# Kernel optimization log

Measured on AMD Instinct MI355X. Metric: run time of the kernel, lower is better.

The kernel has to match this reference:

```python
import jax, jax.numpy as jnp
import numpy as np
from jax import lax

EPS = 1e-5

def _conv3x3(x, w, stride=1):
    # x: [B,C,H,W], w: [O,I,3,3]
    dn = lax.conv_dimension_numbers(x.shape, w.shape, ('NCHW', 'OIHW', 'NCHW'))
    return lax.conv_general_dilated(x, w, window_strides=(stride, stride),
                                    padding=((1, 1), (1, 1)), dimension_numbers=dn)

def _batchnorm(x, gamma, beta):
    # training-mode BN over (N,H,W) per channel
    mean = jnp.mean(x, axis=(0, 2, 3), keepdims=True)
    var = jnp.var(x, axis=(0, 2, 3), keepdims=True)
    inv = lax.rsqrt(var + EPS)
    return (x - mean) * inv * gamma[None, :, None, None] + beta[None, :, None, None]

def setup_inputs() -> dict:
    key = jax.random.key(0)
    ks = jax.random.split(key, 8)
    B, C, H, W, E = 16, 256, 64, 64, 512
    x = jax.random.normal(ks[0], (B, C, H, W), dtype=jnp.float32)
    embedding = jax.random.normal(ks[1], (B, E), dtype=jnp.float32)
    s_conv = 1.0 / np.sqrt(C * 9)
    conv1_w = jax.random.normal(ks[2], (C, C, 3, 3), dtype=jnp.float32) * s_conv
    conv2_w = jax.random.normal(ks[3], (C, C, 3, 3), dtype=jnp.float32) * s_conv
    s_g = 1.0 / np.sqrt(E)
    g1_w = jax.random.normal(ks[4], (E, C), dtype=jnp.float32) * s_g
    g1_b = jnp.zeros((C,), dtype=jnp.float32)
    g2_w = jax.random.normal(ks[5], (E, C), dtype=jnp.float32) * s_g
    g2_b = jnp.zeros((C,), dtype=jnp.float32)
    bn1_g = jnp.ones((C,), dtype=jnp.float32)
    bn1_b = jnp.zeros((C,), dtype=jnp.float32)
    bn2_g = jnp.ones((C,), dtype=jnp.float32)
    bn2_b = jnp.zeros((C,), dtype=jnp.float32)
    return {"x": x, "embedding": embedding, "conv1_w": conv1_w, "conv2_w": conv2_w,
            "g1_w": g1_w, "g1_b": g1_b, "g2_w": g2_w, "g2_b": g2_b,
            "bn1_g": bn1_g, "bn1_b": bn1_b, "bn2_g": bn2_g, "bn2_b": bn2_b}

def reference(x, embedding, conv1_w, conv2_w, g1_w, g1_b, g2_w, g2_b,
              bn1_g, bn1_b, bn2_g, bn2_b):
    identity = x
    # gate 1: per-sample per-channel gate values (softmax over channels)
    gate1 = jax.nn.softmax(embedding @ g1_w + g1_b, axis=-1)  # [B,C]
    out = _conv3x3(x, conv1_w, stride=1) * gate1[:, :, None, None]
    out = jax.nn.relu(_batchnorm(out, bn1_g, bn1_b))
    # gate 2
    gate2 = jax.nn.softmax(embedding @ g2_w + g2_b, axis=-1)  # [B,C]
    out = _conv3x3(out, conv2_w, stride=1) * gate2[:, :, None, None]
    out = _batchnorm(out, bn2_g, bn2_b)
    out = jax.nn.relu(out + identity)
    return (out, gate1, gate2)
```

## Files before the change

kernel.cpp:

```cpp
#include <hip/hip_runtime.h>

typedef __attribute__((ext_vector_type(8))) short short8;
typedef __attribute__((ext_vector_type(4))) float f32x4;

#define HP 66

__device__ __forceinline__ unsigned short f2bf(float f) {
  unsigned u = __builtin_bit_cast(unsigned, f);
  u += 0x7FFFu + ((u >> 16) & 1u);
  return (unsigned short)(u >> 16);
}
__device__ __forceinline__ float bf2f(unsigned short h) {
  return __builtin_bit_cast(float, ((unsigned)h) << 16);
}
__device__ __forceinline__ __attribute__((address_space(3))) void* to_as3(void* p) {
  return (__attribute__((address_space(3))) void*)(unsigned)(unsigned long long)p;
}
__device__ __forceinline__ const __attribute__((address_space(1))) void* to_as1(const void* p) {
  return (const __attribute__((address_space(1))) void*)(unsigned long long)p;
}

#define SB0() __builtin_amdgcn_sched_barrier(0)
#define BAR() do { SB0(); __builtin_amdgcn_s_barrier(); SB0(); } while (0)

__global__ __launch_bounds__(256) void k_prep(
    const float* __restrict__ x, unsigned short* __restrict__ xp,
    const float* __restrict__ w1, const float* __restrict__ w2,
    unsigned short* __restrict__ wT1, unsigned short* __restrict__ wT2,
    const float* __restrict__ emb,
    const float* __restrict__ g1w, const float* __restrict__ g1b,
    const float* __restrict__ g2w, const float* __restrict__ g2b,
    float* __restrict__ gate1, float* __restrict__ gate2) {
  __shared__ float tile[32][65];
  __shared__ float ebuf[512];
  __shared__ float red[8];
  const int blk = blockIdx.x;
  const int t = threadIdx.x;

  if (blk < 8192) {
    int ct = blk & 7, h = (blk >> 3) & 63, b = blk >> 9;
    int c0 = ct * 32;
    int w = t & 63, cs = t >> 6;
#pragma unroll
    for (int i = 0; i < 8; ++i) {
      int c = cs + i * 4;
      tile[c][w] = x[(((b * 256) + c0 + c) * 64 + h) * 64 + w];
    }
    __syncthreads();
    int cl = (t & 15) * 2, w0 = t >> 4;
#pragma unroll
    for (int i = 0; i < 4; ++i) {
      int ww = w0 + i * 16;
      unsigned v = (unsigned)f2bf(tile[cl][ww]) | ((unsigned)f2bf(tile[cl + 1][ww]) << 16);
      *(unsigned*)(xp + ((long)((b*HP + h + 1)*HP + (ww + 1)) * 256 + c0 + cl)) = v;
    }
  } else if (blk < 10272) {
    unsigned u = (unsigned)(blk - 8192) * 256 + t;
    unsigned p_idx = u >> 7, word = u & 127;
    int img = p_idx / 260, p = p_idx % 260;
    int h, w;
    if (p < 66)      { h = 0;  w = p; }
    else if (p < 132){ h = 65; w = p - 66; }
    else             { int q = p - 132; h = 1 + (q >> 1); w = (q & 1) * 65; }
    ((unsigned*)xp)[((long)((img*HP + h)*HP + w) * 256) / 2 + word] = 0u;
  } else if (blk < 10784) {
    int idx = blk - 10272;
    const float* w = (idx >> 8) ? w2 : w1;
    unsigned short* wT = (idx >> 8) ? wT2 : wT1;
    int co = idx & 255;
#pragma unroll
    for (int kk = 0; kk < 9; ++kk)
      wT[co * 2304 + kk * 256 + t] = f2bf(w[(co * 256 + t) * 9 + kk]);
  } else {
    int idx = blk - 10784;
    int b = idx & 15;
    const float* gw = (idx >> 4) ? g2w : g1w;
    const float* gbias = (idx >> 4) ? g2b : g1b;
    float* gout = (idx >> 4) ? gate2 : gate1;
    ebuf[t] = emb[b * 512 + t];
    ebuf[t + 256] = emb[b * 512 + t + 256];
    __syncthreads();
    float acc = gbias[t];
    for (int k = 0; k < 512; ++k) acc += ebuf[k] * gw[k * 256 + t];
    float mx = acc;
    for (int off = 32; off >= 1; off >>= 1) mx = fmaxf(mx, __shfl_xor(mx, off));
    if ((t & 63) == 0) red[t >> 6] = mx;
    __syncthreads();
    mx = fmaxf(fmaxf(red[0], red[1]), fmaxf(red[2], red[3]));
    float e = expf(acc - mx);
    float sm = e;
    for (int off = 32; off >= 1; off >>= 1) sm += __shfl_xor(sm, off);
    if ((t & 63) == 0) red[4 + (t >> 6)] = sm;
    __syncthreads();
    sm = red[4] + red[5] + red[6] + red[7];
    gout[b * 256 + t] = e / sm;
  }
}

__global__ __launch_bounds__(512, 2) void k_conv(
    const unsigned short* __restrict__ inp,
    const unsigned short* __restrict__ wT,
    const float* __restrict__ gate,
    unsigned short* __restrict__ yout,
    float* __restrict__ partials) {
  __shared__ short As[2][256][64];
  __shared__ short Bs[2][256][64];
  __shared__ float sbuf[2][256][2];

  const int t = threadIdx.x;
  const int lane = t & 63;
  const int wid = t >> 6;
  const int wm = wid >> 2;
  const int wn = wid & 3;
  const int lr = lane & 15;
  const int hi = lane >> 4;
  const int key = lr & 7;

  const int blk = ((blockIdx.x & 7) << 5) + (blockIdx.x >> 3);
  const int b = blk >> 4;
  const int hh4 = (blk & 15) << 2;

  const int r0 = t >> 3;
  const int cdst = (t & 7) << 3;
  const int cg8 = (((t & 7) ^ ((t >> 3) & 7)) << 3);

  int aoff[4];
#pragma unroll
  for (int i = 0; i < 4; ++i)
    aoff[i] = (b * HP + hh4 + i) * HP + r0;

  auto stageA = [&](int buf, int half, int s) {
    int kk = s >> 2;
    int kh = (kk * 11) >> 5;
    int khw = kh * 66 + (kk - kh * 3);
    int ci = ((s & 3) << 6) + cg8;
    const unsigned short* g0 = inp + (long)(aoff[half * 2 + 0] + khw) * 256 + ci;
    const unsigned short* g1 = inp + (long)(aoff[half * 2 + 1] + khw) * 256 + ci;
    __builtin_amdgcn_global_load_lds(to_as1(g0), to_as3((void*)&As[buf][half * 128 + r0][cdst]), 16, 0, 0);
    __builtin_amdgcn_global_load_lds(to_as1(g1), to_as3((void*)&As[buf][half * 128 + 64 + r0][cdst]), 16, 0, 0);
  };
  auto stageB = [&](int buf, int half, int s) {
    int co0 = half * 128 + r0;
    const unsigned short* g0 = wT + (long)co0 * 2304 + s * 64 + cg8;
    const unsigned short* g1 = wT + (long)(co0 + 64) * 2304 + s * 64 + cg8;
    __builtin_amdgcn_global_load_lds(to_as1(g0), to_as3((void*)&Bs[buf][half * 128 + r0][cdst]), 16, 0, 0);
    __builtin_amdgcn_global_load_lds(to_as1(g1), to_as3((void*)&Bs[buf][half * 128 + 64 + r0][cdst]), 16, 0, 0);
  };

  f32x4 acc[8][4];
#pragma unroll
  for (int i = 0; i < 8; ++i)
#pragma unroll
    for (int j = 0; j < 4; ++j) acc[i][j] = (f32x4){0.f, 0.f, 0.f, 0.f};

  short8 afrag0[4][2], afrag1[4][2];
  short8 bfrag0[2][2], bfrag1[2][2];

#define RD_A(ARR, MH, BUF)                                                           \
  _Pragma("unroll") for (int mf = 0; mf < 4; ++mf)                                   \
    _Pragma("unroll") for (int ks = 0; ks < 2; ++ks)                                 \
      ARR[mf][ks] = *(const short8*)&As[BUF][wm * 128 + ((MH) * 4 + mf) * 16 + lr][((ks * 4 + hi) ^ key) << 3];
#define RD_B(ARR, NH, BUF)                                                           \
  _Pragma("unroll") for (int nf = 0; nf < 2; ++nf)                                   \
    _Pragma("unroll") for (int ks = 0; ks < 2; ++ks)                                 \
      ARR[nf][ks] = *(const short8*)&Bs[BUF][wn * 64 + ((NH) * 2 + nf) * 16 + lr][((ks * 4 + hi) ^ key) << 3];

#define QUADQ(AF, BF, mh, nh)                                                        \
  do {                                                                               \
    __builtin_amdgcn_s_setprio(1);                                                   \
    _Pragma("unroll") for (int ks = 0; ks < 2; ++ks)                                 \
      _Pragma("unroll") for (int mo = 0; mo < 4; ++mo)                               \
        _Pragma("unroll") for (int no = 0; no < 2; ++no)                             \
          acc[(mh) * 4 + mo][(nh) * 2 + no] = __builtin_amdgcn_mfma_f32_16x16x32_bf16( \
              AF[mo][ks], BF[no][ks], acc[(mh) * 4 + mo][(nh) * 2 + no], 0, 0, 0);   \
    __builtin_amdgcn_s_setprio(0);                                                   \
  } while (0)

  stageA(0, 0, 0); stageB(0, 0, 0); stageA(0, 1, 0); stageB(0, 1, 0);
  stageA(1, 0, 1); stageB(1, 0, 1); stageA(1, 1, 1); stageB(1, 1, 1);
  asm volatile("s_waitcnt vmcnt(8)" ::: "memory");
  BAR();
  RD_B(bfrag0, 0, 0);
  RD_A(afrag0, 0, 0);

#define KTHALF2(SEL, kt)                                                             \
  {                                                                                  \
    RD_B(bfrag1, 1, SEL);                                                            \
    RD_A(afrag1, 1, SEL);                                                            \
    SB0();                                                                           \
    QUADQ(afrag0, bfrag0, 0, 0);                                                     \
    QUADQ(afrag0, bfrag1, 0, 1);                                                     \
    QUADQ(afrag1, bfrag0, 1, 0);                                                     \
    if ((kt) < 35) { asm volatile("s_waitcnt vmcnt(4)" ::: "memory"); }              \
    BAR();                                                                           \
    if ((kt) < 35) { RD_B(bfrag0, 0, SEL ^ 1); RD_A(afrag0, 0, SEL ^ 1); }           \
    if ((kt) + 2 < 36) { stageA(SEL, 0, (kt) + 2); stageB(SEL, 0, (kt) + 2);         \
                         stageA(SEL, 1, (kt) + 2); stageB(SEL, 1, (kt) + 2); }       \
    SB0();                                                                           \
    QUADQ(afrag1, bfrag1, 1, 1);                                                     \
    if ((kt) < 34)      { asm volatile("s_waitcnt vmcnt(8)" ::: "memory"); }         \
    else if ((kt) == 34){ asm volatile("s_waitcnt vmcnt(0)" ::: "memory"); }         \
    BAR();                                                                           \
  }

  for (int i = 0; i < 18; ++i) {
    const int kt0 = 2 * i;
    KTHALF2(0, kt0)
    KTHALF2(1, kt0 + 1)
  }
#undef KTHALF2
#undef QUADQ
#undef RD_A
#undef RD_B

  float g[4];
#pragma unroll
  for (int nf = 0; nf < 4; ++nf) g[nf] = gate[(b << 8) + wn * 64 + nf * 16 + lr];

  float s[4] = {0, 0, 0, 0}, sq[4] = {0, 0, 0, 0};
  const int mrow0 = (blk << 8) + wm * 128 + (hi << 2);
  const int c0 = wn * 64 + lr;
#pragma unroll
  for (int mf = 0; mf < 8; ++mf)
#pragma unroll
    for (int r = 0; r < 4; ++r) {
      const int mm = mrow0 + mf * 16 + r;
#pragma unroll
      for (int nf = 0; nf < 4; ++nf) {
        float v = acc[mf][nf][r] * g[nf];
        yout[(long)mm * 256 + c0 + nf * 16] = f2bf(v);
        s[nf] += v;
        sq[nf] += v * v;
      }
    }
#pragma unroll
  for (int nf = 0; nf < 4; ++nf) {
    s[nf] += __shfl_xor(s[nf], 16);  s[nf] += __shfl_xor(s[nf], 32);
    sq[nf] += __shfl_xor(sq[nf], 16); sq[nf] += __shfl_xor(sq[nf], 32);
  }
  if (hi == 0) {
#pragma unroll
    for (int nf = 0; nf < 4; ++nf) {
      int c = wn * 64 + nf * 16 + lr;
      sbuf[wm][c][0] = s[nf];
      sbuf[wm][c][1] = sq[nf];
    }
  }
  __syncthreads();
  if (t < 256) {
    partials[((blk << 8) + t) * 2]     = sbuf[0][t][0] + sbuf[1][t][0];
    partials[((blk << 8) + t) * 2 + 1] = sbuf[0][t][1] + sbuf[1][t][1];
  }
}

__global__ __launch_bounds__(256) void k_bnfin(const float* __restrict__ partials,
                                               const float* __restrict__ gamma,
                                               const float* __restrict__ beta,
                                               float2* __restrict__ aff) {
  __shared__ float red[8];
  int c = blockIdx.x, t = threadIdx.x;
  float s = partials[(t * 256 + c) * 2];
  float sq = partials[(t * 256 + c) * 2 + 1];
  for (int off = 32; off >= 1; off >>= 1) { s += __shfl_xor(s, off); sq += __shfl_xor(sq, off); }
  if ((t & 63) == 0) { red[t >> 6] = s; red[4 + (t >> 6)] = sq; }
  __syncthreads();
  if (t == 0) {
    s = red[0] + red[1] + red[2] + red[3];
    sq = red[4] + red[5] + red[6] + red[7];
    float mean = s * (1.0f / 65536.0f);
    float var = fmaxf(sq * (1.0f / 65536.0f) - mean * mean, 0.0f);
    float inv = rsqrtf(var + 1e-5f);
    float ga = gamma[c] * inv;
    aff[c] = make_float2(ga, beta[c] - mean * ga);
  }
}

__global__ __launch_bounds__(256) void k_mid(const unsigned short* __restrict__ y1,
                                             const float2* __restrict__ aff,
                                             unsigned short* __restrict__ zp) {
  long idx = (long)blockIdx.x * 256 + threadIdx.x;
  int c0 = (int)(idx & 31) * 8;
  long pos = idx >> 5;
  int b = (int)(pos >> 12), hw = (int)(pos & 4095);
  int h = hw >> 6, w = hw & 63;
  uint4 v = *(const uint4*)(y1 + pos * 256 + c0);
  unsigned vv[4] = {v.x, v.y, v.z, v.w};
  unsigned outp[4];
#pragma unroll
  for (int j = 0; j < 4; ++j) {
    float2 aL = aff[c0 + 2 * j], aH = aff[c0 + 2 * j + 1];
    float lo = fmaxf(aL.x * bf2f((unsigned short)(vv[j] & 0xFFFF)) + aL.y, 0.f);
    float hiv = fmaxf(aH.x * bf2f((unsigned short)(vv[j] >> 16)) + aH.y, 0.f);
    outp[j] = (unsigned)f2bf(lo) | ((unsigned)f2bf(hiv) << 16);
  }
  unsigned short* dst = zp + (long)((b * HP + h + 1) * HP + w + 1) * 256 + c0;
  *(uint4*)dst = make_uint4(outp[0], outp[1], outp[2], outp[3]);
}

__global__ __launch_bounds__(256) void k_final(const unsigned short* __restrict__ y2,
                                               const float2* __restrict__ aff,
                                               const float* __restrict__ x,
                                               float* __restrict__ out) {
  __shared__ float tile[64][33];
  int blk = blockIdx.x;
  int ct = blk & 7, h = (blk >> 3) & 63, b = blk >> 9;
  int c0 = ct * 32;
  int t = threadIdx.x;
  int cl = (t & 15) * 2, w0 = t >> 4;
#pragma unroll
  for (int i = 0; i < 4; ++i) {
    int w = w0 + i * 16;
    unsigned v = *(const unsigned*)(y2 + (long)((b * 4096) + h * 64 + w) * 256 + c0 + cl);
    float2 aL = aff[c0 + cl], aH = aff[c0 + cl + 1];
    tile[w][cl] = aL.x * bf2f((unsigned short)(v & 0xFFFF)) + aL.y;
    tile[w][cl + 1] = aH.x * bf2f((unsigned short)(v >> 16)) + aH.y;
  }
  __syncthreads();
  int w = t & 63, csub = t >> 6;
#pragma unroll
  for (int j = 0; j < 8; ++j) {
    int c = c0 + csub * 8 + j;
    long o = ((long)(b * 256 + c) * 64 + h) * 64 + w;
    out[o] = fmaxf(tile[w][csub * 8 + j] + x[o], 0.f);
  }
}

extern "C" void kernel_launch(void* const* d_in, const int* in_sizes, int n_in,
                              void* d_out, int out_size, void* d_ws, size_t ws_size,
                              hipStream_t stream) {
  const float* x    = (const float*)d_in[0];
  const float* emb  = (const float*)d_in[1];
  const float* w1   = (const float*)d_in[2];
  const float* w2   = (const float*)d_in[3];
  const float* g1w  = (const float*)d_in[4];
  const float* g1b  = (const float*)d_in[5];
  const float* g2w  = (const float*)d_in[6];
  const float* g2b  = (const float*)d_in[7];
  const float* bn1g = (const float*)d_in[8];
  const float* bn1b = (const float*)d_in[9];
  const float* bn2g = (const float*)d_in[10];
  const float* bn2b = (const float*)d_in[11];

  float* out = (float*)d_out;
  float* gate1 = out + 16777216;
  float* gate2 = gate1 + 4096;

  char* ws = (char*)d_ws;
  const size_t OFF_XP  = 0;
  const size_t OFF_WT1 = 35684352;
  const size_t OFF_WT2 = OFF_WT1 + 1179648;
  const size_t OFF_Y   = OFF_WT2 + 1179648;
  const size_t OFF_PART = OFF_Y + 33554432;
  const size_t OFF_AFF1 = OFF_PART + 1048576;
  const size_t OFF_AFF2 = OFF_AFF1 + 2048;

  unsigned short* xp  = (unsigned short*)(ws + OFF_XP);
  unsigned short* wT1 = (unsigned short*)(ws + OFF_WT1);
  unsigned short* wT2 = (unsigned short*)(ws + OFF_WT2);
  unsigned short* y   = (unsigned short*)(ws + OFF_Y);
  float* part = (float*)(ws + OFF_PART);
  float2* aff1 = (float2*)(ws + OFF_AFF1);
  float2* aff2 = (float2*)(ws + OFF_AFF2);

  k_prep<<<10816, 256, 0, stream>>>(x, xp, w1, w2, wT1, wT2, emb,
                                    g1w, g1b, g2w, g2b, gate1, gate2);

  k_conv<<<256, 512, 0, stream>>>(xp, wT1, gate1, y, part);
  k_bnfin<<<256, 256, 0, stream>>>(part, bn1g, bn1b, aff1);
  k_mid<<<8192, 256, 0, stream>>>(y, aff1, xp);

  k_conv<<<256, 512, 0, stream>>>(xp, wT2, gate2, y, part);
  k_bnfin<<<256, 256, 0, stream>>>(part, bn2g, bn2b, aff2);
  k_final<<<8192, 256, 0, stream>>>(y, aff2, x, out);
}
```

Before: 213.5 us.

## Restructure GEMM main loop into barrier-separated phases with interleaved staging

Replaces the two-half K-tile loop with an eight-phase schedule per pair of K-steps. Each phase reads one quadrant's fragments, issues part of the next stage's global-to-LDS loads, then runs 16 MFMAs, with a barrier and an lgkmcnt wait between phases. The A and B staging is remapped by row halves so that each load only overwrites LDS rows already consumed in earlier phases. A single A-fragment buffer replaces the double buffer to lower register use. The intent is finer overlap of loads and LDS reads with MFMA work, at the cost of many more barriers and stricter lockstep between waves.

Measured after the change: 216.6 us. No clear change (+1.4%).

```diff
diff --git a/kernel.cpp b/kernel.cpp
--- a/kernel.cpp
+++ b/kernel.cpp
@@ -129,22 +129,22 @@
   for (int i = 0; i < 4; ++i)
     aoff[i] = (b * HP + hh4 + i) * HP + r0;
 
-  auto stageA = [&](int buf, int half, int s) {
+  auto stageA_h = [&](int buf, int h, int s) {
     int kk = s >> 2;
     int kh = (kk * 11) >> 5;
     int khw = kh * 66 + (kk - kh * 3);
     int ci = ((s & 3) << 6) + cg8;
-    const unsigned short* g0 = inp + (long)(aoff[half * 2 + 0] + khw) * 256 + ci;
-    const unsigned short* g1 = inp + (long)(aoff[half * 2 + 1] + khw) * 256 + ci;
-    __builtin_amdgcn_global_load_lds(to_as1(g0), to_as3((void*)&As[buf][half * 128 + r0][cdst]), 16, 0, 0);
-    __builtin_amdgcn_global_load_lds(to_as1(g1), to_as3((void*)&As[buf][half * 128 + 64 + r0][cdst]), 16, 0, 0);
+    const unsigned short* g0 = inp + (long)(aoff[h] + khw) * 256 + ci;
+    const unsigned short* g1 = inp + (long)(aoff[h + 2] + khw) * 256 + ci;
+    __builtin_amdgcn_global_load_lds(to_as1(g0), to_as3((void*)&As[buf][h * 64 + r0][cdst]), 16, 0, 0);
+    __builtin_amdgcn_global_load_lds(to_as1(g1), to_as3((void*)&As[buf][h * 64 + 128 + r0][cdst]), 16, 0, 0);
   };
-  auto stageB = [&](int buf, int half, int s) {
-    int co0 = half * 128 + r0;
-    const unsigned short* g0 = wT + (long)co0 * 2304 + s * 64 + cg8;
-    const unsigned short* g1 = wT + (long)(co0 + 64) * 2304 + s * 64 + cg8;
-    __builtin_amdgcn_global_load_lds(to_as1(g0), to_as3((void*)&Bs[buf][half * 128 + r0][cdst]), 16, 0, 0);
-    __builtin_amdgcn_global_load_lds(to_as1(g1), to_as3((void*)&Bs[buf][half * 128 + 64 + r0][cdst]), 16, 0, 0);
+  auto stageB_h = [&](int buf, int h, int s) {
+    int rB = (r0 & 31) + ((r0 >> 5) << 6) + h * 32;
+    const unsigned short* g0 = wT + (long)rB * 2304 + s * 64 + cg8;
+    const unsigned short* g1 = wT + (long)(rB + 128) * 2304 + s * 64 + cg8;
+    __builtin_amdgcn_global_load_lds(to_as1(g0), to_as3((void*)&Bs[buf][rB][cdst]), 16, 0, 0);
+    __builtin_amdgcn_global_load_lds(to_as1(g1), to_as3((void*)&Bs[buf][rB + 128][cdst]), 16, 0, 0);
   };
 
   f32x4 acc[8][4];
@@ -153,62 +153,82 @@
 #pragma unroll
     for (int j = 0; j < 4; ++j) acc[i][j] = (f32x4){0.f, 0.f, 0.f, 0.f};
 
-  short8 afrag0[4][2], afrag1[4][2];
+  short8 afrag[4][2];
   short8 bfrag0[2][2], bfrag1[2][2];
 
-#define RD_A(ARR, MH, BUF)                                                           \
+#define RD_A(MH, BUF)                                                                \
   _Pragma("unroll") for (int mf = 0; mf < 4; ++mf)                                   \
     _Pragma("unroll") for (int ks = 0; ks < 2; ++ks)                                 \
-      ARR[mf][ks] = *(const short8*)&As[BUF][wm * 128 + ((MH) * 4 + mf) * 16 + lr][((ks * 4 + hi) ^ key) << 3];
+      afrag[mf][ks] = *(const short8*)&As[BUF][wm * 128 + (MH) * 64 + mf * 16 + lr][((ks * 4 + hi) ^ key) << 3];
 #define RD_B(ARR, NH, BUF)                                                           \
   _Pragma("unroll") for (int nf = 0; nf < 2; ++nf)                                   \
     _Pragma("unroll") for (int ks = 0; ks < 2; ++ks)                                 \
       ARR[nf][ks] = *(const short8*)&Bs[BUF][wn * 64 + ((NH) * 2 + nf) * 16 + lr][((ks * 4 + hi) ^ key) << 3];
 
-#define QUADQ(AF, BF, mh, nh)                                                        \
+#define QUADQ(BF, mh, nh)                                                            \
   do {                                                                               \
     __builtin_amdgcn_s_setprio(1);                                                   \
     _Pragma("unroll") for (int ks = 0; ks < 2; ++ks)                                 \
       _Pragma("unroll") for (int mo = 0; mo < 4; ++mo)                               \
         _Pragma("unroll") for (int no = 0; no < 2; ++no)                             \
           acc[(mh) * 4 + mo][(nh) * 2 + no] = __builtin_amdgcn_mfma_f32_16x16x32_bf16( \
-              AF[mo][ks], BF[no][ks], acc[(mh) * 4 + mo][(nh) * 2 + no], 0, 0, 0);   \
+              afrag[mo][ks], BF[no][ks], acc[(mh) * 4 + mo][(nh) * 2 + no], 0, 0, 0); \
     __builtin_amdgcn_s_setprio(0);                                                   \
   } while (0)
 
-  stageA(0, 0, 0); stageB(0, 0, 0); stageA(0, 1, 0); stageB(0, 1, 0);
-  stageA(1, 0, 1); stageB(1, 0, 1); stageA(1, 1, 1); stageB(1, 1, 1);
+#define LGKM0() do { asm volatile("s_waitcnt lgkmcnt(0)" ::: "memory"); SB0(); } while (0)
+
+  stageA_h(0, 0, 0); stageB_h(0, 0, 0); stageA_h(0, 1, 0); stageB_h(0, 1, 0);
+  stageA_h(1, 0, 1); stageB_h(1, 0, 1); stageA_h(1, 1, 1); stageB_h(1, 1, 1);
   asm volatile("s_waitcnt vmcnt(8)" ::: "memory");
   BAR();
-  RD_B(bfrag0, 0, 0);
-  RD_A(afrag0, 0, 0);
-
-#define KTHALF2(SEL, kt)                                                             \
-  {                                                                                  \
-    RD_B(bfrag1, 1, SEL);                                                            \
-    RD_A(afrag1, 1, SEL);                                                            \
-    SB0();                                                                           \
-    QUADQ(afrag0, bfrag0, 0, 0);                                                     \
-    QUADQ(afrag0, bfrag1, 0, 1);                                                     \
-    QUADQ(afrag1, bfrag0, 1, 0);                                                     \
-    if ((kt) < 35) { asm volatile("s_waitcnt vmcnt(4)" ::: "memory"); }              \
-    BAR();                                                                           \
-    if ((kt) < 35) { RD_B(bfrag0, 0, SEL ^ 1); RD_A(afrag0, 0, SEL ^ 1); }           \
-    if ((kt) + 2 < 36) { stageA(SEL, 0, (kt) + 2); stageB(SEL, 0, (kt) + 2);         \
-                         stageA(SEL, 1, (kt) + 2); stageB(SEL, 1, (kt) + 2); }       \
-    SB0();                                                                           \
-    QUADQ(afrag1, bfrag1, 1, 1);                                                     \
-    if ((kt) < 34)      { asm volatile("s_waitcnt vmcnt(8)" ::: "memory"); }         \
-    else if ((kt) == 34){ asm volatile("s_waitcnt vmcnt(0)" ::: "memory"); }         \
-    BAR();                                                                           \
-  }
 
   for (int i = 0; i < 18; ++i) {
-    const int kt0 = 2 * i;
-    KTHALF2(0, kt0)
-    KTHALF2(1, kt0 + 1)
-  }
-#undef KTHALF2
+    const int s2 = 2 * i + 2;
+    const int s3 = 2 * i + 3;
+    const bool g2q = (s2 < 36), g3q = (s3 < 36);
+    RD_B(bfrag0, 0, 0);
+    RD_A(0, 0);
+    BAR(); LGKM0();
+    QUADQ(bfrag0, 0, 0);
+    BAR();
+    RD_B(bfrag1, 1, 0);
+    if (g2q) stageA_h(0, 0, s2);
+    BAR(); LGKM0();
+    QUADQ(bfrag1, 0, 1);
+    BAR();
+    RD_A(1, 0);
+    if (g2q) stageB_h(0, 0, s2);
+    BAR(); LGKM0();
+    QUADQ(bfrag1, 1, 1);
+    BAR();
+    if (g2q) { stageA_h(0, 1, s2); stageB_h(0, 1, s2); }
+    BAR(); LGKM0();
+    QUADQ(bfrag0, 1, 0);
+    asm volatile("s_waitcnt vmcnt(8)" ::: "memory");
+    BAR();
+    RD_B(bfrag0, 0, 1);
+    RD_A(0, 1);
+    BAR(); LGKM0();
+    QUADQ(bfrag0, 0, 0);
+    BAR();
+    RD_B(bfrag1, 1, 1);
+    if (g3q) stageA_h(1, 0, s3);
+    BAR(); LGKM0();
+    QUADQ(bfrag1, 0, 1);
+    BAR();
+    RD_A(1, 1);
+    if (g3q) stageB_h(1, 0, s3);
+    BAR(); LGKM0();
+    QUADQ(bfrag1, 1, 1);
+    BAR();
+    if (g3q) { stageA_h(1, 1, s3); stageB_h(1, 1, s3); }
+    BAR(); LGKM0();
+    QUADQ(bfrag0, 1, 0);
+    asm volatile("s_waitcnt vmcnt(8)" ::: "memory");
+    BAR();
+  }
+#undef LGKM0
 #undef QUADQ
 #undef RD_A
 #undef RD_B
```

## Shrink conv tiles to 128x128 with 256-thread blocks and 1024-block grid

Applied to the files above, without the earlier changes.

Implicit-GEMM conv tile changes from 256x256 per 512-thread block to 128x128 per 256-thread block, splitting output channels into two halves. The grid grows from 256 to 1024 blocks. This is meant to fill all 256 CUs with several blocks each instead of one block per CU, which should improve latency hiding and occupancy. The partials layout is rearranged into separate sum and sum-of-squares planes, and the BN finalize kernel now reduces 512 tiles. The trade-off is that the smaller tiles reuse less data, so each block does more global and LDS traffic per FLOP.

Result: slower. 238.1 us (+11.5%).

```diff
diff --git a/kernel.cpp b/kernel.cpp
--- a/kernel.cpp
+++ b/kernel.cpp
@@ -97,28 +97,30 @@
   }
 }
 
-__global__ __launch_bounds__(512, 2) void k_conv(
+__global__ __launch_bounds__(256, 2) void k_conv(
     const unsigned short* __restrict__ inp,
     const unsigned short* __restrict__ wT,
     const float* __restrict__ gate,
     unsigned short* __restrict__ yout,
     float* __restrict__ partials) {
-  __shared__ short As[2][256][64];
-  __shared__ short Bs[2][256][64];
-  __shared__ float sbuf[2][256][2];
+  __shared__ short As[2][128][64];
+  __shared__ short Bs[2][128][64];
+  __shared__ float sbuf[2][128][2];
 
   const int t = threadIdx.x;
   const int lane = t & 63;
   const int wid = t >> 6;
-  const int wm = wid >> 2;
-  const int wn = wid & 3;
+  const int wm = wid >> 1;
+  const int wn = wid & 1;
   const int lr = lane & 15;
   const int hi = lane >> 4;
   const int key = lr & 7;
 
-  const int blk = ((blockIdx.x & 7) << 5) + (blockIdx.x >> 3);
-  const int b = blk >> 4;
-  const int hh4 = (blk & 15) << 2;
+  const int blk = ((blockIdx.x & 7) << 7) + (blockIdx.x >> 3);
+  const int mt = blk >> 1;
+  const int nt = blk & 1;
+  const int b = mt >> 5;
+  const int hh2 = (mt & 31) << 1;
 
   const int r0 = t >> 3;
   const int cdst = (t & 7) << 3;
@@ -127,57 +129,57 @@
   int aoff[4];
 #pragma unroll
   for (int i = 0; i < 4; ++i)
-    aoff[i] = (b * HP + hh4 + i) * HP + r0;
-
-  auto stageA = [&](int buf, int half, int s) {
+    aoff[i] = (b * HP + hh2 + (i >> 1)) * HP + (r0 + 32 * (i & 1));
+
+  auto stageA_h = [&](int buf, int h, int s) {
     int kk = s >> 2;
     int kh = (kk * 11) >> 5;
     int khw = kh * 66 + (kk - kh * 3);
     int ci = ((s & 3) << 6) + cg8;
-    const unsigned short* g0 = inp + (long)(aoff[half * 2 + 0] + khw) * 256 + ci;
-    const unsigned short* g1 = inp + (long)(aoff[half * 2 + 1] + khw) * 256 + ci;
-    __builtin_amdgcn_global_load_lds(to_as1(g0), to_as3((void*)&As[buf][half * 128 + r0][cdst]), 16, 0, 0);
-    __builtin_amdgcn_global_load_lds(to_as1(g1), to_as3((void*)&As[buf][half * 128 + 64 + r0][cdst]), 16, 0, 0);
+    const unsigned short* g0 = inp + (long)(aoff[h] + khw) * 256 + ci;
+    const unsigned short* g1 = inp + (long)(aoff[2 + h] + khw) * 256 + ci;
+    __builtin_amdgcn_global_load_lds(to_as1(g0), to_as3((void*)&As[buf][h * 32 + r0][cdst]), 16, 0, 0);
+    __builtin_amdgcn_global_load_lds(to_as1(g1), to_as3((void*)&As[buf][64 + h * 32 + r0][cdst]), 16, 0, 0);
   };
-  auto stageB = [&](int buf, int half, int s) {
-    int co0 = half * 128 + r0;
-    const unsigned short* g0 = wT + (long)co0 * 2304 + s * 64 + cg8;
-    const unsigned short* g1 = wT + (long)(co0 + 64) * 2304 + s * 64 + cg8;
-    __builtin_amdgcn_global_load_lds(to_as1(g0), to_as3((void*)&Bs[buf][half * 128 + r0][cdst]), 16, 0, 0);
-    __builtin_amdgcn_global_load_lds(to_as1(g1), to_as3((void*)&Bs[buf][half * 128 + 64 + r0][cdst]), 16, 0, 0);
+  auto stageB_h = [&](int buf, int h, int s) {
+    int co = nt * 128 + h * 32 + r0;
+    const unsigned short* g0 = wT + (long)co * 2304 + s * 64 + cg8;
+    const unsigned short* g1 = wT + (long)(co + 64) * 2304 + s * 64 + cg8;
+    __builtin_amdgcn_global_load_lds(to_as1(g0), to_as3((void*)&Bs[buf][h * 32 + r0][cdst]), 16, 0, 0);
+    __builtin_amdgcn_global_load_lds(to_as1(g1), to_as3((void*)&Bs[buf][64 + h * 32 + r0][cdst]), 16, 0, 0);
   };
 
-  f32x4 acc[8][4];
-#pragma unroll
-  for (int i = 0; i < 8; ++i)
+  f32x4 acc[4][4];
+#pragma unroll
+  for (int i = 0; i < 4; ++i)
 #pragma unroll
     for (int j = 0; j < 4; ++j) acc[i][j] = (f32x4){0.f, 0.f, 0.f, 0.f};
 
-  short8 afrag0[4][2], afrag1[4][2];
+  short8 afrag0[2][2], afrag1[2][2];
   short8 bfrag0[2][2], bfrag1[2][2];
 
-#define RD_A(ARR, MH, BUF)                                                           \
-  _Pragma("unroll") for (int mf = 0; mf < 4; ++mf)                                   \
+#define RD_A(ARR, AH, BUF)                                                           \
+  _Pragma("unroll") for (int mf = 0; mf < 2; ++mf)                                   \
     _Pragma("unroll") for (int ks = 0; ks < 2; ++ks)                                 \
-      ARR[mf][ks] = *(const short8*)&As[BUF][wm * 128 + ((MH) * 4 + mf) * 16 + lr][((ks * 4 + hi) ^ key) << 3];
+      ARR[mf][ks] = *(const short8*)&As[BUF][wm * 64 + (AH) * 32 + mf * 16 + lr][((ks * 4 + hi) ^ key) << 3];
 #define RD_B(ARR, NH, BUF)                                                           \
   _Pragma("unroll") for (int nf = 0; nf < 2; ++nf)                                   \
     _Pragma("unroll") for (int ks = 0; ks < 2; ++ks)                                 \
-      ARR[nf][ks] = *(const short8*)&Bs[BUF][wn * 64 + ((NH) * 2 + nf) * 16 + lr][((ks * 4 + hi) ^ key) << 3];
+      ARR[nf][ks] = *(const short8*)&Bs[BUF][wn * 64 + (NH) * 32 + nf * 16 + lr][((ks * 4 + hi) ^ key) << 3];
 
 #define QUADQ(AF, BF, mh, nh)                                                        \
   do {                                                                               \
     __builtin_amdgcn_s_setprio(1);                                                   \
     _Pragma("unroll") for (int ks = 0; ks < 2; ++ks)                                 \
-      _Pragma("unroll") for (int mo = 0; mo < 4; ++mo)                               \
+      _Pragma("unroll") for (int mo = 0; mo < 2; ++mo)                               \
         _Pragma("unroll") for (int no = 0; no < 2; ++no)                             \
-          acc[(mh) * 4 + mo][(nh) * 2 + no] = __builtin_amdgcn_mfma_f32_16x16x32_bf16( \
-              AF[mo][ks], BF[no][ks], acc[(mh) * 4 + mo][(nh) * 2 + no], 0, 0, 0);   \
+          acc[(mh) * 2 + mo][(nh) * 2 + no] = __builtin_amdgcn_mfma_f32_16x16x32_bf16( \
+              AF[mo][ks], BF[no][ks], acc[(mh) * 2 + mo][(nh) * 2 + no], 0, 0, 0);   \
     __builtin_amdgcn_s_setprio(0);                                                   \
   } while (0)
 
-  stageA(0, 0, 0); stageB(0, 0, 0); stageA(0, 1, 0); stageB(0, 1, 0);
-  stageA(1, 0, 1); stageB(1, 0, 1); stageA(1, 1, 1); stageB(1, 1, 1);
+  stageA_h(0, 0, 0); stageB_h(0, 0, 0); stageA_h(0, 1, 0); stageB_h(0, 1, 0);
+  stageA_h(1, 0, 1); stageB_h(1, 0, 1); stageA_h(1, 1, 1); stageB_h(1, 1, 1);
   asm volatile("s_waitcnt vmcnt(8)" ::: "memory");
   BAR();
   RD_B(bfrag0, 0, 0);
@@ -194,8 +196,8 @@
     if ((kt) < 35) { asm volatile("s_waitcnt vmcnt(4)" ::: "memory"); }              \
     BAR();                                                                           \
     if ((kt) < 35) { RD_B(bfrag0, 0, SEL ^ 1); RD_A(afrag0, 0, SEL ^ 1); }           \
-    if ((kt) + 2 < 36) { stageA(SEL, 0, (kt) + 2); stageB(SEL, 0, (kt) + 2);         \
-                         stageA(SEL, 1, (kt) + 2); stageB(SEL, 1, (kt) + 2); }       \
+    if ((kt) + 2 < 36) { stageA_h(SEL, 0, (kt) + 2); stageB_h(SEL, 0, (kt) + 2);     \
+                         stageA_h(SEL, 1, (kt) + 2); stageB_h(SEL, 1, (kt) + 2); }   \
     SB0();                                                                           \
     QUADQ(afrag1, bfrag1, 1, 1);                                                     \
     if ((kt) < 34)      { asm volatile("s_waitcnt vmcnt(8)" ::: "memory"); }         \
@@ -215,13 +217,14 @@
 
   float g[4];
 #pragma unroll
-  for (int nf = 0; nf < 4; ++nf) g[nf] = gate[(b << 8) + wn * 64 + nf * 16 + lr];
+  for (int nf = 0; nf < 4; ++nf)
+    g[nf] = gate[(b << 8) + nt * 128 + wn * 64 + nf * 16 + lr];
 
   float s[4] = {0, 0, 0, 0}, sq[4] = {0, 0, 0, 0};
-  const int mrow0 = (blk << 8) + wm * 128 + (hi << 2);
-  const int c0 = wn * 64 + lr;
-#pragma unroll
-  for (int mf = 0; mf < 8; ++mf)
+  const int mrow0 = mt * 128 + wm * 64 + (hi << 2);
+  const int c0 = nt * 128 + wn * 64 + lr;
+#pragma unroll
+  for (int mf = 0; mf < 4; ++mf)
 #pragma unroll
     for (int r = 0; r < 4; ++r) {
       const int mm = mrow0 + mf * 16 + r;
@@ -247,9 +250,9 @@
     }
   }
   __syncthreads();
-  if (t < 256) {
-    partials[((blk << 8) + t) * 2]     = sbuf[0][t][0] + sbuf[1][t][0];
-    partials[((blk << 8) + t) * 2 + 1] = sbuf[0][t][1] + sbuf[1][t][1];
+  if (t < 128) {
+    partials[mt * 256 + nt * 128 + t]          = sbuf[0][t][0] + sbuf[1][t][0];
+    partials[131072 + mt * 256 + nt * 128 + t] = sbuf[0][t][1] + sbuf[1][t][1];
   }
 }
 
@@ -259,8 +262,8 @@
                                                float2* __restrict__ aff) {
   __shared__ float red[8];
   int c = blockIdx.x, t = threadIdx.x;
-  float s = partials[(t * 256 + c) * 2];
-  float sq = partials[(t * 256 + c) * 2 + 1];
+  float s  = partials[t * 256 + c]          + partials[(t + 256) * 256 + c];
+  float sq = partials[131072 + t * 256 + c] + partials[131072 + (t + 256) * 256 + c];
   for (int off = 32; off >= 1; off >>= 1) { s += __shfl_xor(s, off); sq += __shfl_xor(sq, off); }
   if ((t & 63) == 0) { red[t >> 6] = s; red[4 + (t >> 6)] = sq; }
   __syncthreads();
@@ -351,7 +354,7 @@
   const size_t OFF_WT2 = OFF_WT1 + 1179648;
   const size_t OFF_Y   = OFF_WT2 + 1179648;
   const size_t OFF_PART = OFF_Y + 33554432;
-  const size_t OFF_AFF1 = OFF_PART + 1048576;
+  const size_t OFF_AFF1 = OFF_PART + 2097152;
   const size_t OFF_AFF2 = OFF_AFF1 + 2048;
 
   unsigned short* xp  = (unsigned short*)(ws + OFF_XP);
@@ -365,11 +368,11 @@
   k_prep<<<10816, 256, 0, stream>>>(x, xp, w1, w2, wT1, wT2, emb,
                                     g1w, g1b, g2w, g2b, gate1, gate2);
 
-  k_conv<<<256, 512, 0, stream>>>(xp, wT1, gate1, y, part);
+  k_conv<<<1024, 256, 0, stream>>>(xp, wT1, gate1, y, part);
   k_bnfin<<<256, 256, 0, stream>>>(part, bn1g, bn1b, aff1);
   k_mid<<<8192, 256, 0, stream>>>(y, aff1, xp);
 
-  k_conv<<<256, 512, 0, stream>>>(xp, wT2, gate2, y, part);
+  k_conv<<<1024, 256, 0, stream>>>(xp, wT2, gate2, y, part);
   k_bnfin<<<256, 256, 0, stream>>>(part, bn2g, bn2b, aff2);
   k_final<<<8192, 256, 0, stream>>>(y, aff2, x, out);
 }
```
